# Kernel tuning notes

Measured on AMD Instinct MI355X. Metric: run time of the kernel, lower is better.

The kernel has to match this reference:

```python
import jax, jax.numpy as jnp
import numpy as np

NF = 128  # latent_dim / number of filters


def setup_inputs() -> dict:
    key = jax.random.key(0)
    k1, k2, k3, k4 = jax.random.split(key, 4)
    B, H, W, C = 4, 64, 64, 128
    x = jax.random.normal(k1, (B, H, W, C), dtype=jnp.float32)
    y = jax.random.normal(k2, (B, H, W, C), dtype=jnp.float32)
    # 1x1 conv kernels (C_in, C_out) + biases, glorot-ish scale
    scale = 1.0 / np.sqrt(C)
    W1 = jax.random.normal(k3, (C, NF), dtype=jnp.float32) * scale
    W2 = jax.random.normal(k4, (C, NF), dtype=jnp.float32) * scale
    b1 = jnp.zeros((NF,), dtype=jnp.float32)
    b2 = jnp.zeros((NF,), dtype=jnp.float32)
    return {"x": x, "y": y, "W1": W1, "b1": b1, "W2": W2, "b2": b2}


def reference(x, y, W1, b1, W2, b2):
    B, H, Wd, C = x.shape
    hw = H * Wd
    # 1x1 convs == per-pixel matmul
    xq = jnp.einsum('bhwc,cf->bhwf', x, W1) + b1   # conv1(x)
    yk = jnp.einsum('bhwc,cf->bhwf', y, W2) + b2   # conv2(y)
    xq_r = xq.reshape(B, hw, NF)
    yk_r = yk.reshape(B, hw, NF)
    # A_ij = sigmoid(y_i . x_j), full (hw x hw) sigmoid attention
    A = jax.nn.sigmoid(jnp.einsum('bic,bjc->bij', yk_r, xq_r))
    out = jnp.einsum('bij,bjc->bic', A, yk_r).reshape(B, H, Wd, NF)
    # residual add of the *projected* x (matches original: x was overwritten by conv1)
    out = out + xq
    return out
```

## Files before the change

### kernel.cpp

```cpp
#include <hip/hip_runtime.h>
#include <hip/hip_bf16.h>
#include <stdint.h>

typedef float f32x16 __attribute__((ext_vector_type(16)));
typedef float f32x4  __attribute__((ext_vector_type(4)));
typedef short s16x8  __attribute__((ext_vector_type(8)));
typedef unsigned int u32x4 __attribute__((ext_vector_type(4)));

#define HWSZ   4096
#define NBATCH 4
#define LOG2E  1.44269504088896340736f

__device__ __forceinline__ unsigned short f2bf(float f) {
    unsigned u = __builtin_bit_cast(unsigned, f);
    u += 0x7FFFu + ((u >> 16) & 1u);
    return (unsigned short)(u >> 16);
}
__device__ __forceinline__ unsigned cvt_pk_bf16(float lo, float hi) {
    __hip_bfloat162 h = __float22bfloat162_rn(make_float2(lo, hi));
    return *reinterpret_cast<unsigned*>(&h);
}
__device__ __forceinline__ float sigm2(float s) {
    return __builtin_amdgcn_rcpf(1.f + __builtin_amdgcn_exp2f(-s));
}
// ... 91 lines not shown
            for (int rg = 0; rg < 4; ++rg) {
                float p0 = acc[ft][4 * rg + 0] + bias_v[ft];
                float p1 = acc[ft][4 * rg + 1] + bias_v[ft];
                float p2 = acc[ft][4 * rg + 2] + bias_v[ft];
                float p3 = acc[ft][4 * rg + 3] + bias_v[ft];
                int jb = 8 * rg + 4 * g;
                *(uint2*)&Tlds[f][jb] = make_uint2(cvt_pk_bf16(p0, p1), cvt_pk_bf16(p2, p3));
                size_t o = (size_t)(r0 + jb) * 128 + f;
                yk_bf[o]       = f2bf(p0);
                yk_bf[o + 128] = f2bf(p1);
                yk_bf[o + 256] = f2bf(p2);
                yk_bf[o + 384] = f2bf(p3);
            }
        }
    }
    __syncthreads();

    {
        int f  = t >> 1;
        int jh = (t & 1) * 16;
        unsigned short* dst = ykT_bf + ((size_t)(b * 128 + f)) * HWSZ + j0 + jh;
        #pragma unroll
        for (int c = 0; c < 2; ++c)
            *(s16x8*)(dst + c * 8) = *(const s16x8*)&Tlds[f][jh + c * 8];
    }
}

#define KT_STR   136
#define VT_STR   72
#define KT_BYTES (64 * KT_STR * 2)
#define VT_BYTES (128 * VT_STR * 2)
#define BUF_BYTES (KT_BYTES + VT_BYTES)

__global__ __launch_bounds__(256, 2) void attn128_kernel(
    const unsigned short* __restrict__ Kbf,
    const unsigned short* __restrict__ Qbf,
    const unsigned short* __restrict__ Vtbf,
    unsigned* __restrict__ outp)
{
    __shared__ __align__(16) char smem[2 * BUF_BYTES];

    const int t    = threadIdx.x;
    const int lane = t & 63;
    const int qt   = t >> 6;
    const int l31  = lane & 31;
    const int g    = lane >> 5;

    const int split  = blockIdx.x >> 7;
    const int r      = blockIdx.x & 127;
    const int b      = r >> 5;
    const int qb     = (r & 31) * 128;
    const int jBegin = split * (HWSZ / 4);
    const int nt     = (HWSZ / 4) / 64;

    s16x8 qfrag[8];
    {
        const unsigned short* qp =
            Qbf + (((size_t)(b * HWSZ + qb + 32 * qt + l31)) << 7) + g * 8;
        #pragma unroll
        for (int fs = 0; fs < 8; ++fs)
            qfrag[fs] = *(const s16x8*)(qp + fs * 16);
    }

    f32x16 acc[4];
    #pragma unroll
    for (int ft = 0; ft < 4; ++ft)
        #pragma unroll
        for (int i = 0; i < 16; ++i) acc[ft][i] = 0.f;

    f32x16 zv;
    #pragma unroll
    for (int i = 0; i < 16; ++i) zv[i] = 0.f;

    const unsigned short* Kbase = Kbf  + (((size_t)b * HWSZ) << 7);
    const unsigned short* Vbase = Vtbf + (((size_t)b) << 7) * HWSZ;

    const unsigned short* kSrc = Kbase + (size_t)(jBegin + (t >> 4)) * 128 + (t & 15) * 8;
    const unsigned short* vSrc = Vbase + (size_t)(t >> 3) * HWSZ + jBegin + (t & 7) * 8;
    const int kDst = (t >> 4) * KT_STR + (t & 15) * 8;
    const int vDst = (t >> 3) * VT_STR + (t & 7) * 8;

    {
        unsigned short* Kl = (unsigned short*)smem;
        unsigned short* Vl = (unsigned short*)(smem + KT_BYTES);
        #pragma unroll
        for (int i = 0; i < 4; ++i)
            *(s16x8*)(Kl + kDst + i * 16 * KT_STR) = *(const s16x8*)(kSrc + (size_t)i * 2048);
        #pragma unroll
        for (int i = 0; i < 4; ++i)
            *(s16x8*)(Vl + vDst + i * 32 * VT_STR) = *(const s16x8*)(vSrc + (size_t)i * 32 * HWSZ);
    }
    __syncthreads();

    int c = 0;
    for (int it = 0; it < nt; ++it) {
        const bool pre = (it + 1 < nt);
        const unsigned short* Kl = (const unsigned short*)(smem + c * BUF_BYTES);
        const unsigned short* Vl = (const unsigned short*)(smem + c * BUF_BYTES + KT_BYTES);

        s16x8 kf0[8], kf1[8];
        {
            const unsigned short* Krow = Kl + (size_t)l31 * KT_STR + g * 8;
            #pragma unroll
            for (int fs = 0; fs < 8; ++fs)
                kf0[fs] = *(const s16x8*)(Krow + fs * 16);
        }
        f32x16 s0a, s0b;
        __builtin_amdgcn_s_setprio(1);
        #pragma unroll
        for (int fs = 0; fs < 4; ++fs) {
            s0a = __builtin_amdgcn_mfma_f32_32x32x16_bf16(kf0[fs],     qfrag[fs],
                      fs == 0 ? zv : s0a, 0, 0, 0);
            s0b = __builtin_amdgcn_mfma_f32_32x32x16_bf16(kf0[fs + 4], qfrag[fs + 4],
                      fs == 0 ? zv : s0b, 0, 0, 0);
        }
        __builtin_amdgcn_s_setprio(0);

        {
            const unsigned short* Krow = Kl + (size_t)(32 + l31) * KT_STR + g * 8;
            #pragma unroll
            for (int fs = 0; fs < 8; ++fs)
                kf1[fs] = *(const s16x8*)(Krow + fs * 16);
        }
        s16x8 kr[4], vr[4];
        if (pre) {
            kSrc += 64 * 128;
            vSrc += 64;
            #pragma unroll
            for (int i = 0; i < 4; ++i)
                kr[i] = *(const s16x8*)(kSrc + (size_t)i * 2048);
            #pragma unroll
            for (int i = 0; i < 4; ++i)
                vr[i] = *(const s16x8*)(vSrc + (size_t)i * 32 * HWSZ);
        }

        f32x16 s1a, s1b;
        unsigned W0[2][4], W1[2][4];
        #pragma unroll
        for (int fs = 0; fs < 4; ++fs) {
            s1a = __builtin_amdgcn_mfma_f32_32x32x16_bf16(kf1[fs],     qfrag[fs],
                      fs == 0 ? zv : s1a, 0, 0, 0);
            s1b = __builtin_amdgcn_mfma_f32_32x32x16_bf16(kf1[fs + 4], qfrag[fs + 4],
                      fs == 0 ? zv : s1b, 0, 0, 0);
            const int rg = fs;
            float p0 = sigm2(s0a[4 * rg + 0] + s0b[4 * rg + 0]);
            float p1 = sigm2(s0a[4 * rg + 1] + s0b[4 * rg + 1]);
            float p2 = sigm2(s0a[4 * rg + 2] + s0b[4 * rg + 2]);
            float p3 = sigm2(s0a[4 * rg + 3] + s0b[4 * rg + 3]);
            W0[0][rg] = cvt_pk_bf16(p0, p1);
            W1[0][rg] = cvt_pk_bf16(p2, p3);
        }

        __builtin_amdgcn_s_setprio(1);
        #pragma unroll
        for (int s2 = 0; s2 < 2; ++s2) {
            unsigned a0 = W0[0][2 * s2], b0 = W0[0][2 * s2 + 1];
            unsigned a1 = W1[0][2 * s2], b1 = W1[0][2 * s2 + 1];
            asm("v_permlane32_swap_b32 %0, %1" : "+v"(a0), "+v"(b0));
            asm("v_permlane32_swap_b32 %0, %1" : "+v"(a1), "+v"(b1));
            u32x4 pw;
            pw[0] = a0; pw[1] = a1; pw[2] = b0; pw[3] = b1;
            s16x8 pf = __builtin_bit_cast(s16x8, pw);
            #pragma unroll
            for (int ft = 0; ft < 4; ++ft) {
                s16x8 vf = *(const s16x8*)(Vl + (size_t)(32 * ft + l31) * VT_STR + s2 * 16 + g * 8);
                acc[ft] = __builtin_amdgcn_mfma_f32_32x32x16_bf16(pf, vf, acc[ft], 0, 0, 0);
            }
            #pragma unroll
            for (int h = 0; h < 2; ++h) {
                const int rg = 2 * s2 + h;
                float p0 = sigm2(s1a[4 * rg + 0] + s1b[4 * rg + 0]);
                float p1 = sigm2(s1a[4 * rg + 1] + s1b[4 * rg + 1]);
                float p2 = sigm2(s1a[4 * rg + 2] + s1b[4 * rg + 2]);
                float p3 = sigm2(s1a[4 * rg + 3] + s1b[4 * rg + 3]);
                W0[1][rg] = cvt_pk_bf16(p0, p1);
                W1[1][rg] = cvt_pk_bf16(p2, p3);
            }
        }

        #pragma unroll
        for (int s2 = 0; s2 < 2; ++s2) {
            unsigned a0 = W0[1][2 * s2], b0 = W0[1][2 * s2 + 1];
            unsigned a1 = W1[1][2 * s2], b1 = W1[1][2 * s2 + 1];
            asm("v_permlane32_swap_b32 %0, %1" : "+v"(a0), "+v"(b0));
            asm("v_permlane32_swap_b32 %0, %1" : "+v"(a1), "+v"(b1));
            u32x4 pw;
            pw[0] = a0; pw[1] = a1; pw[2] = b0; pw[3] = b1;
            s16x8 pf = __builtin_bit_cast(s16x8, pw);
            const int ks = 2 + s2;
            #pragma unroll
            for (int ft = 0; ft < 4; ++ft) {
                s16x8 vf = *(const s16x8*)(Vl + (size_t)(32 * ft + l31) * VT_STR + ks * 16 + g * 8);
                acc[ft] = __builtin_amdgcn_mfma_f32_32x32x16_bf16(pf, vf, acc[ft], 0, 0, 0);
            }
        }
        __builtin_amdgcn_s_setprio(0);

        if (pre) {
            unsigned short* Kd = (unsigned short*)(smem + (c ^ 1) * BUF_BYTES);
            unsigned short* Vd = (unsigned short*)(smem + (c ^ 1) * BUF_BYTES + KT_BYTES);
            #pragma unroll
            for (int i = 0; i < 4; ++i)
                *(s16x8*)(Kd + kDst + i * 16 * KT_STR) = kr[i];
            #pragma unroll
            for (int i = 0; i < 4; ++i)
                *(s16x8*)(Vd + vDst + i * 32 * VT_STR) = vr[i];
        }
        __syncthreads();
        c ^= 1;
    }

    unsigned* op = outp + (size_t)split * ((size_t)NBATCH * HWSZ * 64);
    #pragma unroll
    for (int ft = 0; ft < 4; ++ft)
    #pragma unroll
    for (int pr = 0; pr < 8; ++pr) {
        int r2 = 2 * pr;
        int row = (r2 & 3) + 8 * (r2 >> 2) + 4 * g;
        int q = qb + 32 * qt + row;
        unsigned v = cvt_pk_bf16(acc[ft][r2], acc[ft][r2 + 1]);
        op[((size_t)(b * HWSZ + q) >> 1) * 128 + 32 * ft + l31] = v;
    }
}

template<bool SPLIT>
__global__ __launch_bounds__(256, 2) void attn_kernel(
    const unsigned short* __restrict__ Kbf,
    const unsigned short* __restrict__ Qbf,
    const unsigned short* __restrict__ Vtbf,
    const float* __restrict__ resid,
    float* __restrict__ outp)
{
    __shared__ __align__(16) char smem[2 * BUF_BYTES];

    const int t    = threadIdx.x;
    const int lane = t & 63;
    const int w    = t >> 6;
    const int qt   = w & 1;
    const int jt   = w >> 1;
    const int l31  = lane & 31;
    const int g    = lane >> 5;

    int bid = blockIdx.x;
    int half = 0;
    if (SPLIT) { half = bid >> 8; bid &= 255; }
    const int b      = bid >> 6;
    const int qb     = (bid & 63) * 64;
    const int jBegin = half * (HWSZ / 2);
    const int nt     = (SPLIT ? HWSZ / 2 : HWSZ) / 64;

    s16x8 qfrag[8];
    {
        const unsigned short* qp =
            Qbf + (((size_t)(b * HWSZ + qb + 32 * qt + l31)) << 7) + g * 8;
        #pragma unroll
        for (int fs = 0; fs < 8; ++fs)
            qfrag[fs] = *(const s16x8*)(qp + fs * 16);
    }

    f32x16 acc[4];
    #pragma unroll
    for (int ft = 0; ft < 4; ++ft)
        #pragma unroll
        for (int i = 0; i < 16; ++i) acc[ft][i] = 0.f;

    const unsigned short* Kbase = Kbf  + (((size_t)b * HWSZ) << 7);
    const unsigned short* Vbase = Vtbf + (((size_t)b) << 7) * HWSZ;

    const unsigned short* kSrc = Kbase + (size_t)(jBegin + (t >> 4)) * 128 + (t & 15) * 8;
    const unsigned short* vSrc = Vbase + (size_t)(t >> 3) * HWSZ + jBegin + (t & 7) * 8;
    const int kDst = (t >> 4) * KT_STR + (t & 15) * 8;
    const int vDst = (t >> 3) * VT_STR + (t & 7) * 8;

    {
        unsigned short* Kl = (unsigned short*)smem;
        unsigned short* Vl = (unsigned short*)(smem + KT_BYTES);
        #pragma unroll
        for (int i = 0; i < 4; ++i)
            *(s16x8*)(Kl + kDst + i * 16 * KT_STR) = *(const s16x8*)(kSrc + (size_t)i * 2048);
        #pragma unroll
        for (int i = 0; i < 4; ++i)
            *(s16x8*)(Vl + vDst + i * 32 * VT_STR) = *(const s16x8*)(vSrc + (size_t)i * 32 * HWSZ);
    }
    __syncthreads();

    int c = 0;
    for (int it = 0; it < nt; ++it) {
        const bool pre = (it + 1 < nt);
        s16x8 kr[4], vr[4];
        if (pre) {
            kSrc += 64 * 128;
            vSrc += 64;
            #pragma unroll
            for (int i = 0; i < 4; ++i)
                kr[i] = *(const s16x8*)(kSrc + (size_t)i * 2048);
            #pragma unroll
            for (int i = 0; i < 4; ++i)
                vr[i] = *(const s16x8*)(vSrc + (size_t)i * 32 * HWSZ);
        }

        const unsigned short* Kl = (const unsigned short*)(smem + c * BUF_BYTES);
        const unsigned short* Vl = (const unsigned short*)(smem + c * BUF_BYTES + KT_BYTES);

        f32x16 sa, sb;
        #pragma unroll
        for (int i = 0; i < 16; ++i) { sa[i] = 0.f; sb[i] = 0.f; }
        const unsigned short* Krow = Kl + (size_t)(32 * jt + l31) * KT_STR + g * 8;
        __builtin_amdgcn_s_setprio(1);
        #pragma unroll
        for (int fs = 0; fs < 4; ++fs) {
            sa = __builtin_amdgcn_mfma_f32_32x32x16_bf16(
                     *(const s16x8*)(Krow + fs * 16), qfrag[fs], sa, 0, 0, 0);
            sb = __builtin_amdgcn_mfma_f32_32x32x16_bf16(
                     *(const s16x8*)(Krow + (fs + 4) * 16), qfrag[fs + 4], sb, 0, 0, 0);
        }
        __builtin_amdgcn_s_setprio(0);

        unsigned W0[4], W1[4];
        #pragma unroll
        for (int rg = 0; rg < 4; ++rg) {
            float p0 = sigm2(sa[4 * rg + 0] + sb[4 * rg + 0]);
            float p1 = sigm2(sa[4 * rg + 1] + sb[4 * rg + 1]);
            float p2 = sigm2(sa[4 * rg + 2] + sb[4 * rg + 2]);
            float p3 = sigm2(sa[4 * rg + 3] + sb[4 * rg + 3]);
            W0[rg] = cvt_pk_bf16(p0, p1);
            W1[rg] = cvt_pk_bf16(p2, p3);
        }

        #pragma unroll
        for (int s2 = 0; s2 < 2; ++s2) {
            unsigned a0 = W0[2 * s2], b0 = W0[2 * s2 + 1];
            unsigned a1 = W1[2 * s2], b1 = W1[2 * s2 + 1];
            asm("v_permlane32_swap_b32 %0, %1" : "+v"(a0), "+v"(b0));
            asm("v_permlane32_swap_b32 %0, %1" : "+v"(a1), "+v"(b1));
            u32x4 pw;
            pw[0] = a0; pw[1] = a1; pw[2] = b0; pw[3] = b1;
            s16x8 pf = __builtin_bit_cast(s16x8, pw);
            const int ks = 2 * jt + s2;
            __builtin_amdgcn_s_setprio(1);
            #pragma unroll
            for (int ft = 0; ft < 4; ++ft) {
                s16x8 vf = *(const s16x8*)(Vl + (size_t)(32 * ft + l31) * VT_STR + ks * 16 + g * 8);
                acc[ft] = __builtin_amdgcn_mfma_f32_32x32x16_bf16(pf, vf, acc[ft], 0, 0, 0);
            }
            __builtin_amdgcn_s_setprio(0);
        }

        if (pre) {
            unsigned short* Kd = (unsigned short*)(smem + (c ^ 1) * BUF_BYTES);
            unsigned short* Vd = (unsigned short*)(smem + (c ^ 1) * BUF_BYTES + KT_BYTES);
            #pragma unroll
            for (int i = 0; i < 4; ++i)
                *(s16x8*)(Kd + kDst + i * 16 * KT_STR) = kr[i];
            #pragma unroll
            for (int i = 0; i < 4; ++i)
                *(s16x8*)(Vd + vDst + i * 32 * VT_STR) = vr[i];
        }
        __syncthreads();
        c ^= 1;
    }

    float* red = (float*)smem;
    if (jt == 1) {
        #pragma unroll
        for (int ft = 0; ft < 4; ++ft)
        #pragma unroll
        for (int r = 0; r < 16; ++r) {
            int row = (r & 3) + 8 * (r >> 2) + 4 * g;
            red[qt * 4096 + row * 128 + 32 * ft + l31] = acc[ft][r];
        }
    }
    __syncthreads();
    if (jt == 0) {
        float* op = outp + (SPLIT ? (size_t)half * ((size_t)NBATCH * HWSZ * 128) : 0);
        #pragma unroll
        for (int ft = 0; ft < 4; ++ft)
        #pragma unroll
        for (int r = 0; r < 16; ++r) {
            int row = (r & 3) + 8 * (r >> 2) + 4 * g;
            float v = acc[ft][r] + red[qt * 4096 + row * 128 + 32 * ft + l31];
            int q = qb + 32 * qt + row;
            size_t o = (((size_t)(b * HWSZ + q)) << 7) + 32 * ft + l31;
            if (SPLIT) op[o] = v;
            else       op[o] = v + resid[o];
        }
    }
}

__global__ __launch_bounds__(256, 1) void reduce2_kernel(
    const float* __restrict__ p0, const float* __restrict__ p1, float* outp)
{
    int i = blockIdx.x * 256 + threadIdx.x;
    f32x4 a = ((const f32x4*)p0)[i];
    f32x4 b = ((const f32x4*)p1)[i];
    f32x4 c = ((f32x4*)outp)[i];
    ((f32x4*)outp)[i] = a + b + c;
}

__global__ __launch_bounds__(256, 1) void reduce4bf_kernel(
    const unsigned* __restrict__ parts, const unsigned short* __restrict__ xqu,
    float* __restrict__ outp)
{
    const size_t NU = (size_t)NBATCH * HWSZ * 64;
    size_t j0 = ((size_t)blockIdx.x * 256 + threadIdx.x) * 4;
    f32x4 lo, hi;
    #pragma unroll
    for (int e = 0; e < 4; ++e) { lo[e] = 0.f; hi[e] = 0.f; }
    #pragma unroll
    for (int k = 0; k < 4; ++k) {
        u32x4 v = *(const u32x4*)(parts + k * NU + j0);
        #pragma unroll
        for (int e = 0; e < 4; ++e) {
            lo[e] += bf_lo(v[e]);
            hi[e] += bf_hi(v[e]);
        }
    }
    size_t p  = j0 >> 7;
    int    f0 = (int)(j0 & 127);
    size_t o0 = (p * 2) * 128 + f0;
    const ushort4 r0 = *(const ushort4*)(xqu + o0);
    const ushort4 r1 = *(const ushort4*)(xqu + o0 + 128);
    lo[0] += bf2f(r0.x); lo[1] += bf2f(r0.y); lo[2] += bf2f(r0.z); lo[3] += bf2f(r0.w);
    hi[0] += bf2f(r1.x); hi[1] += bf2f(r1.y); hi[2] += bf2f(r1.z); hi[3] += bf2f(r1.w);
    *(f32x4*)(outp + o0)       = lo;
    *(f32x4*)(outp + o0 + 128) = hi;
}

extern "C" void kernel_launch(void* const* d_in, const int* in_sizes, int n_in,
                              void* d_out, int out_size, void* d_ws, size_t ws_size,
                              hipStream_t stream) {
    const float* x  = (const float*)d_in[0];
    const float* y  = (const float*)d_in[1];
    const float* W1 = (const float*)d_in[2];
    const float* b1 = (const float*)d_in[3];
    const float* W2 = (const float*)d_in[4];
    const float* b2 = (const float*)d_in[5];
    float* out = (float*)d_out;

    const size_t NELEM = (size_t)NBATCH * HWSZ * 128;
    unsigned short* xq_bf  = (unsigned short*)d_ws;
    unsigned short* yk_bf  = xq_bf + NELEM;
    unsigned short* ykT_bf = yk_bf + NELEM;
    unsigned short* xqu_bf = ykT_bf + NELEM;
    unsigned* partu = (unsigned*)(xqu_bf + NELEM);
    float* part = (float*)(ykT_bf + NELEM);

    if (ws_size >= NELEM * 16) {
        proj_kernel<false><<<(int)(NBATCH * HWSZ / 32), 256, 0, stream>>>(
            x, y, W1, b1, W2, b2, nullptr, xqu_bf, xq_bf, yk_bf, ykT_bf);
        attn128_kernel<<<512, 256, 0, stream>>>(xq_bf, yk_bf, ykT_bf, partu);
        reduce4bf_kernel<<<(int)(NELEM / 2048), 256, 0, stream>>>(partu, xqu_bf, out);
    } else if (ws_size >= NELEM * 14) {
        proj_kernel<true><<<(int)(NBATCH * HWSZ / 32), 256, 0, stream>>>(
            x, y, W1, b1, W2, b2, out, nullptr, xq_bf, yk_bf, ykT_bf);
        attn_kernel<true><<<512, 256, 0, stream>>>(xq_bf, yk_bf, ykT_bf, out, part);
        reduce2_kernel<<<(int)(NELEM / 1024), 256, 0, stream>>>(part, part + NELEM, out);
    } else {
        proj_kernel<true><<<(int)(NBATCH * HWSZ / 32), 256, 0, stream>>>(
            x, y, W1, b1, W2, b2, out, nullptr, xq_bf, yk_bf, ykT_bf);
        attn_kernel<false><<<256, 256, 0, stream>>>(xq_bf, yk_bf, ykT_bf, out, out);
    }
}
```

Measured before the change: 60.83 us.

## Process two query sub-tiles per wave in attention kernel to reuse K/V fragments

The 128-query attention block moves from four waves with one 32-row query tile each to two waves with two 32-row query tiles each. Each K fragment and V fragment read from LDS now feeds two MFMA chains, halving LDS reads per unit of work, and the S/sigmoid stages are interleaved across four score tiles to overlap exp with matrix ops. The cost is roughly double the accumulator and fragment registers per wave, a launch bound of one block, and half as many waves to hide latency, which may lower occupancy.

```diff
diff --git a/kernel.cpp b/kernel.cpp
--- a/kernel.cpp
+++ b/kernel.cpp
@@ -147,7 +147,7 @@
 #define VT_BYTES (128 * VT_STR * 2)
 #define BUF_BYTES (KT_BYTES + VT_BYTES)
 
-__global__ __launch_bounds__(256, 2) void attn128_kernel(
+__global__ __launch_bounds__(128, 1) void attn128w2_kernel(
     const unsigned short* __restrict__ Kbf,
     const unsigned short* __restrict__ Qbf,
     const unsigned short* __restrict__ Vtbf,
@@ -157,7 +157,7 @@
 
     const int t    = threadIdx.x;
     const int lane = t & 63;
-    const int qt   = t >> 6;
+    const int wv   = t >> 6;
     const int l31  = lane & 31;
     const int g    = lane >> 5;
 
@@ -168,20 +168,23 @@
     const int jBegin = split * (HWSZ / 4);
     const int nt     = (HWSZ / 4) / 64;
 
-    s16x8 qfrag[8];
-    {
+    s16x8 qfrag[2][8];
+    #pragma unroll
+    for (int qs = 0; qs < 2; ++qs) {
         const unsigned short* qp =
-            Qbf + (((size_t)(b * HWSZ + qb + 32 * qt + l31)) << 7) + g * 8;
+            Qbf + (((size_t)(b * HWSZ + qb + 64 * wv + 32 * qs + l31)) << 7) + g * 8;
         #pragma unroll
         for (int fs = 0; fs < 8; ++fs)
-            qfrag[fs] = *(const s16x8*)(qp + fs * 16);
-    }
-
-    f32x16 acc[4];
-    #pragma unroll
-    for (int ft = 0; ft < 4; ++ft)
-        #pragma unroll
-        for (int i = 0; i < 16; ++i) acc[ft][i] = 0.f;
+            qfrag[qs][fs] = *(const s16x8*)(qp + fs * 16);
+    }
+
+    f32x16 acc[2][4];
+    #pragma unroll
+    for (int qs = 0; qs < 2; ++qs)
+        #pragma unroll
+        for (int ft = 0; ft < 4; ++ft)
+            #pragma unroll
+            for (int i = 0; i < 16; ++i) acc[qs][ft][i] = 0.f;
 
     f32x16 zv;
     #pragma unroll
@@ -199,11 +202,11 @@
         unsigned short* Kl = (unsigned short*)smem;
         unsigned short* Vl = (unsigned short*)(smem + KT_BYTES);
         #pragma unroll
-        for (int i = 0; i < 4; ++i)
-            *(s16x8*)(Kl + kDst + i * 16 * KT_STR) = *(const s16x8*)(kSrc + (size_t)i * 2048);
-        #pragma unroll
-        for (int i = 0; i < 4; ++i)
-            *(s16x8*)(Vl + vDst + i * 32 * VT_STR) = *(const s16x8*)(vSrc + (size_t)i * 32 * HWSZ);
+        for (int i = 0; i < 8; ++i)
+            *(s16x8*)(Kl + kDst + i * 8 * KT_STR) = *(const s16x8*)(kSrc + (size_t)i * 1024);
+        #pragma unroll
+        for (int i = 0; i < 8; ++i)
+            *(s16x8*)(Vl + vDst + i * 16 * VT_STR) = *(const s16x8*)(vSrc + (size_t)i * 16 * HWSZ);
     }
     __syncthreads();
 
@@ -213,6 +216,8 @@
         const unsigned short* Kl = (const unsigned short*)(smem + c * BUF_BYTES);
         const unsigned short* Vl = (const unsigned short*)(smem + c * BUF_BYTES + KT_BYTES);
 
+        unsigned Wlo[2][2][4], Whi[2][2][4];
+
         s16x8 kf0[8], kf1[8];
         {
             const unsigned short* Krow = Kl + (size_t)l31 * KT_STR + g * 8;
@@ -220,14 +225,14 @@
             for (int fs = 0; fs < 8; ++fs)
                 kf0[fs] = *(const s16x8*)(Krow + fs * 16);
         }
-        f32x16 s0a, s0b;
+        f32x16 s00a, s00b;
         __builtin_amdgcn_s_setprio(1);
         #pragma unroll
         for (int fs = 0; fs < 4; ++fs) {
-            s0a = __builtin_amdgcn_mfma_f32_32x32x16_bf16(kf0[fs],     qfrag[fs],
-                      fs == 0 ? zv : s0a, 0, 0, 0);
-            s0b = __builtin_amdgcn_mfma_f32_32x32x16_bf16(kf0[fs + 4], qfrag[fs + 4],
-                      fs == 0 ? zv : s0b, 0, 0, 0);
+            s00a = __builtin_amdgcn_mfma_f32_32x32x16_bf16(kf0[fs],     qfrag[0][fs],
+                       fs == 0 ? zv : s00a, 0, 0, 0);
+            s00b = __builtin_amdgcn_mfma_f32_32x32x16_bf16(kf0[fs + 4], qfrag[0][fs + 4],
+                       fs == 0 ? zv : s00b, 0, 0, 0);
         }
         __builtin_amdgcn_s_setprio(0);
 
@@ -237,76 +242,119 @@
             for (int fs = 0; fs < 8; ++fs)
                 kf1[fs] = *(const s16x8*)(Krow + fs * 16);
         }
-        s16x8 kr[4], vr[4];
+        s16x8 kr[8], vr[8];
         if (pre) {
             kSrc += 64 * 128;
             vSrc += 64;
             #pragma unroll
-            for (int i = 0; i < 4; ++i)
-                kr[i] = *(const s16x8*)(kSrc + (size_t)i * 2048);
-            #pragma unroll
-            for (int i = 0; i < 4; ++i)
-                vr[i] = *(const s16x8*)(vSrc + (size_t)i * 32 * HWSZ);
-        }
-
-        f32x16 s1a, s1b;
-        unsigned W0[2][4], W1[2][4];
+            for (int i = 0; i < 8; ++i)
+                kr[i] = *(const s16x8*)(kSrc + (size_t)i * 1024);
+            #pragma unroll
+            for (int i = 0; i < 8; ++i)
+                vr[i] = *(const s16x8*)(vSrc + (size_t)i * 16 * HWSZ);
+        }
+
+        f32x16 s01a, s01b;
         #pragma unroll
         for (int fs = 0; fs < 4; ++fs) {
-            s1a = __builtin_amdgcn_mfma_f32_32x32x16_bf16(kf1[fs],     qfrag[fs],
-                      fs == 0 ? zv : s1a, 0, 0, 0);
-            s1b = __builtin_amdgcn_mfma_f32_32x32x16_bf16(kf1[fs + 4], qfrag[fs + 4],
-                      fs == 0 ? zv : s1b, 0, 0, 0);
+            s01a = __builtin_amdgcn_mfma_f32_32x32x16_bf16(kf0[fs],     qfrag[1][fs],
+                       fs == 0 ? zv : s01a, 0, 0, 0);
+            s01b = __builtin_amdgcn_mfma_f32_32x32x16_bf16(kf0[fs + 4], qfrag[1][fs + 4],
+                       fs == 0 ? zv : s01b, 0, 0, 0);
             const int rg = fs;
-            float p0 = sigm2(s0a[4 * rg + 0] + s0b[4 * rg + 0]);
-            float p1 = sigm2(s0a[4 * rg + 1] + s0b[4 * rg + 1]);
-            float p2 = sigm2(s0a[4 * rg + 2] + s0b[4 * rg + 2]);
-            float p3 = sigm2(s0a[4 * rg + 3] + s0b[4 * rg + 3]);
-            W0[0][rg] = cvt_pk_bf16(p0, p1);
-            W1[0][rg] = cvt_pk_bf16(p2, p3);
+            float p0 = sigm2(s00a[4 * rg + 0] + s00b[4 * rg + 0]);
+            float p1 = sigm2(s00a[4 * rg + 1] + s00b[4 * rg + 1]);
+            float p2 = sigm2(s00a[4 * rg + 2] + s00b[4 * rg + 2]);
+            float p3 = sigm2(s00a[4 * rg + 3] + s00b[4 * rg + 3]);
+            Wlo[0][0][rg] = cvt_pk_bf16(p0, p1);
+            Whi[0][0][rg] = cvt_pk_bf16(p2, p3);
+        }
+
+        f32x16 s10a, s10b;
+        #pragma unroll
+        for (int fs = 0; fs < 4; ++fs) {
+            s10a = __builtin_amdgcn_mfma_f32_32x32x16_bf16(kf1[fs],     qfrag[0][fs],
+                       fs == 0 ? zv : s10a, 0, 0, 0);
+            s10b = __builtin_amdgcn_mfma_f32_32x32x16_bf16(kf1[fs + 4], qfrag[0][fs + 4],
+                       fs == 0 ? zv : s10b, 0, 0, 0);
+            const int rg = fs;
+            float p0 = sigm2(s01a[4 * rg + 0] + s01b[4 * rg + 0]);
+            float p1 = sigm2(s01a[4 * rg + 1] + s01b[4 * rg + 1]);
+            float p2 = sigm2(s01a[4 * rg + 2] + s01b[4 * rg + 2]);
+            float p3 = sigm2(s01a[4 * rg + 3] + s01b[4 * rg + 3]);
+            Wlo[0][1][rg] = cvt_pk_bf16(p0, p1);
+            Whi[0][1][rg] = cvt_pk_bf16(p2, p3);
+        }
+
+        f32x16 s11a, s11b;
+        #pragma unroll
+        for (int fs = 0; fs < 4; ++fs) {
+            s11a = __builtin_amdgcn_mfma_f32_32x32x16_bf16(kf1[fs],     qfrag[1][fs],
+                       fs == 0 ? zv : s11a, 0, 0, 0);
+            s11b = __builtin_amdgcn_mfma_f32_32x32x16_bf16(kf1[fs + 4], qfrag[1][fs + 4],
+                       fs == 0 ? zv : s11b, 0, 0, 0);
+            const int rg = fs;
+            float p0 = sigm2(s10a[4 * rg + 0] + s10b[4 * rg + 0]);
+            float p1 = sigm2(s10a[4 * rg + 1] + s10b[4 * rg + 1]);
+            float p2 = sigm2(s10a[4 * rg + 2] + s10b[4 * rg + 2]);
+            float p3 = sigm2(s10a[4 * rg + 3] + s10b[4 * rg + 3]);
+            Wlo[1][0][rg] = cvt_pk_bf16(p0, p1);
+            Whi[1][0][rg] = cvt_pk_bf16(p2, p3);
         }
 
         __builtin_amdgcn_s_setprio(1);
         #pragma unroll
         for (int s2 = 0; s2 < 2; ++s2) {
-            unsigned a0 = W0[0][2 * s2], b0 = W0[0][2 * s2 + 1];
-            unsigned a1 = W1[0][2 * s2], b1 = W1[0][2 * s2 + 1];
+            unsigned a0 = Wlo[0][0][2 * s2], b0 = Wlo[0][0][2 * s2 + 1];
+            unsigned a1 = Whi[0][0][2 * s2], b1 = Whi[0][0][2 * s2 + 1];
             asm("v_permlane32_swap_b32 %0, %1" : "+v"(a0), "+v"(b0));
             asm("v_permlane32_swap_b32 %0, %1" : "+v"(a1), "+v"(b1));
-            u32x4 pw;
-            pw[0] = a0; pw[1] = a1; pw[2] = b0; pw[3] = b1;
-            s16x8 pf = __builtin_bit_cast(s16x8, pw);
+            u32x4 pw0; pw0[0] = a0; pw0[1] = a1; pw0[2] = b0; pw0[3] = b1;
+            s16x8 pf0 = __builtin_bit_cast(s16x8, pw0);
+            unsigned c0 = Wlo[0][1][2 * s2], d0 = Wlo[0][1][2 * s2 + 1];
+            unsigned c1 = Whi[0][1][2 * s2], d1 = Whi[0][1][2 * s2 + 1];
+            asm("v_permlane32_swap_b32 %0, %1" : "+v"(c0), "+v"(d0));
+            asm("v_permlane32_swap_b32 %0, %1" : "+v"(c1), "+v"(d1));
+            u32x4 pw1; pw1[0] = c0; pw1[1] = c1; pw1[2] = d0; pw1[3] = d1;
+            s16x8 pf1 = __builtin_bit_cast(s16x8, pw1);
             #pragma unroll
             for (int ft = 0; ft < 4; ++ft) {
                 s16x8 vf = *(const s16x8*)(Vl + (size_t)(32 * ft + l31) * VT_STR + s2 * 16 + g * 8);
-                acc[ft] = __builtin_amdgcn_mfma_f32_32x32x16_bf16(pf, vf, acc[ft], 0, 0, 0);
+                acc[0][ft] = __builtin_amdgcn_mfma_f32_32x32x16_bf16(pf0, vf, acc[0][ft], 0, 0, 0);
+                acc[1][ft] = __builtin_amdgcn_mfma_f32_32x32x16_bf16(pf1, vf, acc[1][ft], 0, 0, 0);
             }
             #pragma unroll
             for (int h = 0; h < 2; ++h) {
                 const int rg = 2 * s2 + h;
-                float p0 = sigm2(s1a[4 * rg + 0] + s1b[4 * rg + 0]);
-                float p1 = sigm2(s1a[4 * rg + 1] + s1b[4 * rg + 1]);
-                float p2 = sigm2(s1a[4 * rg + 2] + s1b[4 * rg + 2]);
-                float p3 = sigm2(s1a[4 * rg + 3] + s1b[4 * rg + 3]);
-                W0[1][rg] = cvt_pk_bf16(p0, p1);
-                W1[1][rg] = cvt_pk_bf16(p2, p3);
+                float p0 = sigm2(s11a[4 * rg + 0] + s11b[4 * rg + 0]);
+                float p1 = sigm2(s11a[4 * rg + 1] + s11b[4 * rg + 1]);
+                float p2 = sigm2(s11a[4 * rg + 2] + s11b[4 * rg + 2]);
+                float p3 = sigm2(s11a[4 * rg + 3] + s11b[4 * rg + 3]);
+                Wlo[1][1][rg] = cvt_pk_bf16(p0, p1);
+                Whi[1][1][rg] = cvt_pk_bf16(p2, p3);
             }
         }
 
         #pragma unroll
         for (int s2 = 0; s2 < 2; ++s2) {
-            unsigned a0 = W0[1][2 * s2], b0 = W0[1][2 * s2 + 1];
-            unsigned a1 = W1[1][2 * s2], b1 = W1[1][2 * s2 + 1];
+            unsigned a0 = Wlo[1][0][2 * s2], b0 = Wlo[1][0][2 * s2 + 1];
+            unsigned a1 = Whi[1][0][2 * s2], b1 = Whi[1][0][2 * s2 + 1];
             asm("v_permlane32_swap_b32 %0, %1" : "+v"(a0), "+v"(b0));
             asm("v_permlane32_swap_b32 %0, %1" : "+v"(a1), "+v"(b1));
-            u32x4 pw;
-            pw[0] = a0; pw[1] = a1; pw[2] = b0; pw[3] = b1;
-            s16x8 pf = __builtin_bit_cast(s16x8, pw);
+            u32x4 pw0; pw0[0] = a0; pw0[1] = a1; pw0[2] = b0; pw0[3] = b1;
+            s16x8 pf0 = __builtin_bit_cast(s16x8, pw0);
+            unsigned c0 = Wlo[1][1][2 * s2], d0 = Wlo[1][1][2 * s2 + 1];
+            unsigned c1 = Whi[1][1][2 * s2], d1 = Whi[1][1][2 * s2 + 1];
+            asm("v_permlane32_swap_b32 %0, %1" : "+v"(c0), "+v"(d0));
+            asm("v_permlane32_swap_b32 %0, %1" : "+v"(c1), "+v"(d1));
+            u32x4 pw1; pw1[0] = c0; pw1[1] = c1; pw1[2] = d0; pw1[3] = d1;
+            s16x8 pf1 = __builtin_bit_cast(s16x8, pw1);
             const int ks = 2 + s2;
             #pragma unroll
             for (int ft = 0; ft < 4; ++ft) {
                 s16x8 vf = *(const s16x8*)(Vl + (size_t)(32 * ft + l31) * VT_STR + ks * 16 + g * 8);
-                acc[ft] = __builtin_amdgcn_mfma_f32_32x32x16_bf16(pf, vf, acc[ft], 0, 0, 0);
+                acc[0][ft] = __builtin_amdgcn_mfma_f32_32x32x16_bf16(pf0, vf, acc[0][ft], 0, 0, 0);
+                acc[1][ft] = __builtin_amdgcn_mfma_f32_32x32x16_bf16(pf1, vf, acc[1][ft], 0, 0, 0);
             }
         }
         __builtin_amdgcn_s_setprio(0);
@@ -315,25 +363,27 @@
             unsigned short* Kd = (unsigned short*)(smem + (c ^ 1) * BUF_BYTES);
             unsigned short* Vd = (unsigned short*)(smem + (c ^ 1) * BUF_BYTES + KT_BYTES);
             #pragma unroll
-            for (int i = 0; i < 4; ++i)
-                *(s16x8*)(Kd + kDst + i * 16 * KT_STR) = kr[i];
-            #pragma unroll
-            for (int i = 0; i < 4; ++i)
-                *(s16x8*)(Vd + vDst + i * 32 * VT_STR) = vr[i];
+            for (int i = 0; i < 8; ++i)
+                *(s16x8*)(Kd + kDst + i * 8 * KT_STR) = kr[i];
+            #pragma unroll
+            for (int i = 0; i < 8; ++i)
+                *(s16x8*)(Vd + vDst + i * 16 * VT_STR) = vr[i];
         }
         __syncthreads();
         c ^= 1;
     }
 
     unsigned* op = outp + (size_t)split * ((size_t)NBATCH * HWSZ * 64);
+    #pragma unroll
+    for (int qs = 0; qs < 2; ++qs)
     #pragma unroll
     for (int ft = 0; ft < 4; ++ft)
     #pragma unroll
     for (int pr = 0; pr < 8; ++pr) {
         int r2 = 2 * pr;
         int row = (r2 & 3) + 8 * (r2 >> 2) + 4 * g;
-        int q = qb + 32 * qt + row;
-        unsigned v = cvt_pk_bf16(acc[ft][r2], acc[ft][r2 + 1]);
+        int q = qb + 64 * wv + 32 * qs + row;
+        unsigned v = cvt_pk_bf16(acc[qs][ft][r2], acc[qs][ft][r2 + 1]);
         op[((size_t)(b * HWSZ + q) >> 1) * 128 + 32 * ft + l31] = v;
     }
 }
@@ -563,7 +613,7 @@
     if (ws_size >= NELEM * 16) {
         proj_kernel<false><<<(int)(NBATCH * HWSZ / 32), 256, 0, stream>>>(
             x, y, W1, b1, W2, b2, nullptr, xqu_bf, xq_bf, yk_bf, ykT_bf);
-        attn128_kernel<<<512, 256, 0, stream>>>(xq_bf, yk_bf, ykT_bf, partu);
+        attn128w2_kernel<<<512, 128, 0, stream>>>(xq_bf, yk_bf, ykT_bf, partu);
         reduce4bf_kernel<<<(int)(NELEM / 2048), 256, 0, stream>>>(partu, xqu_bf, out);
     } else if (ws_size >= NELEM * 14) {
         proj_kernel<true><<<(int)(NBATCH * HWSZ / 32), 256, 0, stream>>>(
```

New measurement: 68.51 us. 1.13x slower.

## Load K fragments directly from global into registers, dropping K LDS staging

Applied to the files above, without the earlier changes.

K tiles are no longer staged through shared memory. Each wave now reads its K MFMA fragments straight from global memory into registers and prefetches the next tile's fragments mid-iteration. This removes the K writes to LDS and the later LDS reads, and shrinks shared memory to the V buffers only. In exchange, every one of the 4 waves in a block loads the same K data from global memory (4x redundant traffic, relying on L2/cache hits), and holding 16 extra fragment registers raises register pressure and could hurt occupancy at launch_bounds(256,2).

```diff
diff --git a/kernel.cpp b/kernel.cpp
--- a/kernel.cpp
+++ b/kernel.cpp
@@ -153,7 +153,7 @@
     const unsigned short* __restrict__ Vtbf,
     unsigned* __restrict__ outp)
 {
-    __shared__ __align__(16) char smem[2 * BUF_BYTES];
+    __shared__ __align__(16) unsigned short Vlds[2][128 * VT_STR];
 
     const int t    = threadIdx.x;
     const int lane = t & 63;
@@ -190,60 +190,45 @@
     const unsigned short* Kbase = Kbf  + (((size_t)b * HWSZ) << 7);
     const unsigned short* Vbase = Vtbf + (((size_t)b) << 7) * HWSZ;
 
-    const unsigned short* kSrc = Kbase + (size_t)(jBegin + (t >> 4)) * 128 + (t & 15) * 8;
+    const unsigned short* kPtr = Kbase + (size_t)(jBegin + l31) * 128 + g * 8;
+
+    s16x8 kf[16];
+    #pragma unroll
+    for (int jt = 0; jt < 2; ++jt)
+        #pragma unroll
+        for (int fs = 0; fs < 8; ++fs)
+            kf[jt * 8 + fs] = *(const s16x8*)(kPtr + jt * 32 * 128 + fs * 16);
+
     const unsigned short* vSrc = Vbase + (size_t)(t >> 3) * HWSZ + jBegin + (t & 7) * 8;
-    const int kDst = (t >> 4) * KT_STR + (t & 15) * 8;
     const int vDst = (t >> 3) * VT_STR + (t & 7) * 8;
 
     {
-        unsigned short* Kl = (unsigned short*)smem;
-        unsigned short* Vl = (unsigned short*)(smem + KT_BYTES);
         #pragma unroll
         for (int i = 0; i < 4; ++i)
-            *(s16x8*)(Kl + kDst + i * 16 * KT_STR) = *(const s16x8*)(kSrc + (size_t)i * 2048);
-        #pragma unroll
-        for (int i = 0; i < 4; ++i)
-            *(s16x8*)(Vl + vDst + i * 32 * VT_STR) = *(const s16x8*)(vSrc + (size_t)i * 32 * HWSZ);
+            *(s16x8*)(&Vlds[0][0] + vDst + i * 32 * VT_STR) =
+                *(const s16x8*)(vSrc + (size_t)i * 32 * HWSZ);
     }
     __syncthreads();
 
     int c = 0;
     for (int it = 0; it < nt; ++it) {
         const bool pre = (it + 1 < nt);
-        const unsigned short* Kl = (const unsigned short*)(smem + c * BUF_BYTES);
-        const unsigned short* Vl = (const unsigned short*)(smem + c * BUF_BYTES + KT_BYTES);
-
-        s16x8 kf0[8], kf1[8];
-        {
-            const unsigned short* Krow = Kl + (size_t)l31 * KT_STR + g * 8;
-            #pragma unroll
-            for (int fs = 0; fs < 8; ++fs)
-                kf0[fs] = *(const s16x8*)(Krow + fs * 16);
-        }
+        const unsigned short* Vl = &Vlds[c][0];
+
         f32x16 s0a, s0b;
         __builtin_amdgcn_s_setprio(1);
         #pragma unroll
         for (int fs = 0; fs < 4; ++fs) {
-            s0a = __builtin_amdgcn_mfma_f32_32x32x16_bf16(kf0[fs],     qfrag[fs],
+            s0a = __builtin_amdgcn_mfma_f32_32x32x16_bf16(kf[fs],     qfrag[fs],
                       fs == 0 ? zv : s0a, 0, 0, 0);
-            s0b = __builtin_amdgcn_mfma_f32_32x32x16_bf16(kf0[fs + 4], qfrag[fs + 4],
+            s0b = __builtin_amdgcn_mfma_f32_32x32x16_bf16(kf[fs + 4], qfrag[fs + 4],
                       fs == 0 ? zv : s0b, 0, 0, 0);
         }
         __builtin_amdgcn_s_setprio(0);
 
-        {
-            const unsigned short* Krow = Kl + (size_t)(32 + l31) * KT_STR + g * 8;
-            #pragma unroll
-            for (int fs = 0; fs < 8; ++fs)
-                kf1[fs] = *(const s16x8*)(Krow + fs * 16);
-        }
-        s16x8 kr[4], vr[4];
+        s16x8 vr[4];
         if (pre) {
-            kSrc += 64 * 128;
             vSrc += 64;
-            #pragma unroll
-            for (int i = 0; i < 4; ++i)
-                kr[i] = *(const s16x8*)(kSrc + (size_t)i * 2048);
             #pragma unroll
             for (int i = 0; i < 4; ++i)
                 vr[i] = *(const s16x8*)(vSrc + (size_t)i * 32 * HWSZ);
@@ -253,9 +238,9 @@
         unsigned W0[2][4], W1[2][4];
         #pragma unroll
         for (int fs = 0; fs < 4; ++fs) {
-            s1a = __builtin_amdgcn_mfma_f32_32x32x16_bf16(kf1[fs],     qfrag[fs],
+            s1a = __builtin_amdgcn_mfma_f32_32x32x16_bf16(kf[8 + fs],     qfrag[fs],
                       fs == 0 ? zv : s1a, 0, 0, 0);
-            s1b = __builtin_amdgcn_mfma_f32_32x32x16_bf16(kf1[fs + 4], qfrag[fs + 4],
+            s1b = __builtin_amdgcn_mfma_f32_32x32x16_bf16(kf[8 + fs + 4], qfrag[fs + 4],
                       fs == 0 ? zv : s1b, 0, 0, 0);
             const int rg = fs;
             float p0 = sigm2(s0a[4 * rg + 0] + s0b[4 * rg + 0]);
@@ -264,6 +249,15 @@
             float p3 = sigm2(s0a[4 * rg + 3] + s0b[4 * rg + 3]);
             W0[0][rg] = cvt_pk_bf16(p0, p1);
             W1[0][rg] = cvt_pk_bf16(p2, p3);
+        }
+
+        if (pre) {
+            kPtr += 64 * 128;
+            #pragma unroll
+            for (int jt = 0; jt < 2; ++jt)
+                #pragma unroll
+                for (int fs = 0; fs < 8; ++fs)
+                    kf[jt * 8 + fs] = *(const s16x8*)(kPtr + jt * 32 * 128 + fs * 16);
         }
 
         __builtin_amdgcn_s_setprio(1);
@@ -312,14 +306,9 @@
         __builtin_amdgcn_s_setprio(0);
 
         if (pre) {
-            unsigned short* Kd = (unsigned short*)(smem + (c ^ 1) * BUF_BYTES);
-            unsigned short* Vd = (unsigned short*)(smem + (c ^ 1) * BUF_BYTES + KT_BYTES);
             #pragma unroll
             for (int i = 0; i < 4; ++i)
-                *(s16x8*)(Kd + kDst + i * 16 * KT_STR) = kr[i];
-            #pragma unroll
-            for (int i = 0; i < 4; ++i)
-                *(s16x8*)(Vd + vDst + i * 32 * VT_STR) = vr[i];
+                *(s16x8*)(&Vlds[c ^ 1][0] + vDst + i * 32 * VT_STR) = vr[i];
         }
         __syncthreads();
         c ^= 1;
```

New measurement: 86.54 us. +42.3%, slower.

## Add six-way key-split attention kernel with single-buffered LDS and pipelined sigmoid

Applied to the files above, without the earlier changes.

Adds attn6_kernel, which splits the key/value dimension six ways (768 blocks of 11 or 10 tiles) instead of four, and targets three blocks per CU by dropping to a single LDS buffer. Inside the loop it computes the two 32-row score tiles one after the other and overlaps the sigmoid of the first with the score MFMAs of the second. It also overlaps the second sigmoid with the PV MFMAs of the first. The reduce kernel is templated on the split count, and the older fp32 fallback paths are removed. The new path needs a larger workspace, and the extra split adds partial-output traffic in the reduce. The single buffer also adds an extra barrier per tile.

```diff
diff --git a/kernel.cpp b/kernel.cpp
--- a/kernel.cpp
+++ b/kernel.cpp
@@ -147,6 +147,189 @@
 #define VT_BYTES (128 * VT_STR * 2)
 #define BUF_BYTES (KT_BYTES + VT_BYTES)
 
+__global__ __launch_bounds__(256, 3) void attn6_kernel(
+    const unsigned short* __restrict__ Kbf,
+    const unsigned short* __restrict__ Qbf,
+    const unsigned short* __restrict__ Vtbf,
+    unsigned* __restrict__ outp)
+{
+    __shared__ __align__(16) unsigned short Klds[64 * KT_STR];
+    __shared__ __align__(16) unsigned short Vlds[128 * VT_STR];
+
+    const int t    = threadIdx.x;
+    const int lane = t & 63;
+    const int qt   = t >> 6;
+    const int l31  = lane & 31;
+    const int g    = lane >> 5;
+
+    const int split = blockIdx.x >> 7;
+    const int r     = blockIdx.x & 127;
+    const int b     = r >> 5;
+    const int qb    = (r & 31) * 128;
+    const int st    = 11 * split - (split > 4 ? split - 4 : 0);
+    const int nt    = (split >= 4) ? 10 : 11;
+    const int jBegin = st * 64;
+
+    s16x8 qfrag[8];
+    {
+        const unsigned short* qp =
+            Qbf + (((size_t)(b * HWSZ + qb + 32 * qt + l31)) << 7) + g * 8;
+        #pragma unroll
+        for (int fs = 0; fs < 8; ++fs)
+            qfrag[fs] = *(const s16x8*)(qp + fs * 16);
+    }
+
+    f32x16 acc[4];
+    #pragma unroll
+    for (int ft = 0; ft < 4; ++ft)
+        #pragma unroll
+        for (int i = 0; i < 16; ++i) acc[ft][i] = 0.f;
+
+    f32x16 zv;
+    #pragma unroll
+    for (int i = 0; i < 16; ++i) zv[i] = 0.f;
+
+    const unsigned short* Kbase = Kbf  + (((size_t)b * HWSZ) << 7);
+    const unsigned short* Vbase = Vtbf + (((size_t)b) << 7) * HWSZ;
+
+    const unsigned short* kSrc = Kbase + (size_t)(jBegin + (t >> 4)) * 128 + (t & 15) * 8;
+    const unsigned short* vSrc = Vbase + (size_t)(t >> 3) * HWSZ + jBegin + (t & 7) * 8;
+    const int kDst = (t >> 4) * KT_STR + (t & 15) * 8;
+    const int vDst = (t >> 3) * VT_STR + (t & 7) * 8;
+
+    {
+        #pragma unroll
+        for (int i = 0; i < 4; ++i)
+            *(s16x8*)(Klds + kDst + i * 16 * KT_STR) = *(const s16x8*)(kSrc + (size_t)i * 2048);
+        #pragma unroll
+        for (int i = 0; i < 4; ++i)
+            *(s16x8*)(Vlds + vDst + i * 32 * VT_STR) = *(const s16x8*)(vSrc + (size_t)i * 32 * HWSZ);
+    }
+    __syncthreads();
+
+    for (int it = 0; it < nt; ++it) {
+        const bool pre = (it + 1 < nt);
+
+        s16x8 kf0[8], kf1[8];
+        {
+            const unsigned short* Krow = Klds + (size_t)l31 * KT_STR + g * 8;
+            #pragma unroll
+            for (int fs = 0; fs < 8; ++fs)
+                kf0[fs] = *(const s16x8*)(Krow + fs * 16);
+        }
+        f32x16 s0;
+        __builtin_amdgcn_s_setprio(1);
+        #pragma unroll
+        for (int fs = 0; fs < 8; ++fs)
+            s0 = __builtin_amdgcn_mfma_f32_32x32x16_bf16(kf0[fs], qfrag[fs],
+                     fs == 0 ? zv : s0, 0, 0, 0);
+        __builtin_amdgcn_s_setprio(0);
+
+        {
+            const unsigned short* Krow = Klds + (size_t)(32 + l31) * KT_STR + g * 8;
+            #pragma unroll
+            for (int fs = 0; fs < 8; ++fs)
+                kf1[fs] = *(const s16x8*)(Krow + fs * 16);
+        }
+        s16x8 kr[4], vr[4];
+        if (pre) {
+            kSrc += 64 * 128;
+            vSrc += 64;
+            #pragma unroll
+            for (int i = 0; i < 4; ++i)
+                kr[i] = *(const s16x8*)(kSrc + (size_t)i * 2048);
+            #pragma unroll
+            for (int i = 0; i < 4; ++i)
+                vr[i] = *(const s16x8*)(vSrc + (size_t)i * 32 * HWSZ);
+        }
+
+        f32x16 s1;
+        unsigned W0[2][4], W1[2][4];
+        #pragma unroll
+        for (int fs = 0; fs < 8; ++fs) {
+            s1 = __builtin_amdgcn_mfma_f32_32x32x16_bf16(kf1[fs], qfrag[fs],
+                     fs == 0 ? zv : s1, 0, 0, 0);
+            if (fs < 4) {
+                const int rg = fs;
+                float p0 = sigm2(s0[4 * rg + 0]);
+                float p1 = sigm2(s0[4 * rg + 1]);
+                float p2 = sigm2(s0[4 * rg + 2]);
+                float p3 = sigm2(s0[4 * rg + 3]);
+                W0[0][rg] = cvt_pk_bf16(p0, p1);
+                W1[0][rg] = cvt_pk_bf16(p2, p3);
+            }
+        }
+
+        __builtin_amdgcn_s_setprio(1);
+        #pragma unroll
+        for (int s2 = 0; s2 < 2; ++s2) {
+            unsigned a0 = W0[0][2 * s2], b0 = W0[0][2 * s2 + 1];
+            unsigned a1 = W1[0][2 * s2], b1 = W1[0][2 * s2 + 1];
+            asm("v_permlane32_swap_b32 %0, %1" : "+v"(a0), "+v"(b0));
+            asm("v_permlane32_swap_b32 %0, %1" : "+v"(a1), "+v"(b1));
+            u32x4 pw;
+            pw[0] = a0; pw[1] = a1; pw[2] = b0; pw[3] = b1;
+            s16x8 pf = __builtin_bit_cast(s16x8, pw);
+            #pragma unroll
+            for (int ft = 0; ft < 4; ++ft) {
+                s16x8 vf = *(const s16x8*)(Vlds + (size_t)(32 * ft + l31) * VT_STR + s2 * 16 + g * 8);
+                acc[ft] = __builtin_amdgcn_mfma_f32_32x32x16_bf16(pf, vf, acc[ft], 0, 0, 0);
+            }
+            #pragma unroll
+            for (int h = 0; h < 2; ++h) {
+                const int rg = 2 * s2 + h;
+                float p0 = sigm2(s1[4 * rg + 0]);
+                float p1 = sigm2(s1[4 * rg + 1]);
+                float p2 = sigm2(s1[4 * rg + 2]);
+                float p3 = sigm2(s1[4 * rg + 3]);
+                W0[1][rg] = cvt_pk_bf16(p0, p1);
+                W1[1][rg] = cvt_pk_bf16(p2, p3);
+            }
+        }
+
+        #pragma unroll
+        for (int s2 = 0; s2 < 2; ++s2) {
+            unsigned a0 = W0[1][2 * s2], b0 = W0[1][2 * s2 + 1];
+            unsigned a1 = W1[1][2 * s2], b1 = W1[1][2 * s2 + 1];
+            asm("v_permlane32_swap_b32 %0, %1" : "+v"(a0), "+v"(b0));
+            asm("v_permlane32_swap_b32 %0, %1" : "+v"(a1), "+v"(b1));
+            u32x4 pw;
+            pw[0] = a0; pw[1] = a1; pw[2] = b0; pw[3] = b1;
+            s16x8 pf = __builtin_bit_cast(s16x8, pw);
+            const int ks = 2 + s2;
+            #pragma unroll
+            for (int ft = 0; ft < 4; ++ft) {
+                s16x8 vf = *(const s16x8*)(Vlds + (size_t)(32 * ft + l31) * VT_STR + ks * 16 + g * 8);
+                acc[ft] = __builtin_amdgcn_mfma_f32_32x32x16_bf16(pf, vf, acc[ft], 0, 0, 0);
+            }
+        }
+        __builtin_amdgcn_s_setprio(0);
+
+        __syncthreads();
+        if (pre) {
+            #pragma unroll
+            for (int i = 0; i < 4; ++i)
+                *(s16x8*)(Klds + kDst + i * 16 * KT_STR) = kr[i];
+            #pragma unroll
+            for (int i = 0; i < 4; ++i)
+                *(s16x8*)(Vlds + vDst + i * 32 * VT_STR) = vr[i];
+            __syncthreads();
+        }
+    }
+
+    unsigned* op = outp + (size_t)split * ((size_t)NBATCH * HWSZ * 64);
+    #pragma unroll
+    for (int ft = 0; ft < 4; ++ft)
+    #pragma unroll
+    for (int pr = 0; pr < 8; ++pr) {
+        int r2 = 2 * pr;
+        int row = (r2 & 3) + 8 * (r2 >> 2) + 4 * g;
+        int q = qb + 32 * qt + row;
+        unsigned v = cvt_pk_bf16(acc[ft][r2], acc[ft][r2 + 1]);
+        op[((size_t)(b * HWSZ + q) >> 1) * 128 + 32 * ft + l31] = v;
+    }
+}
+
 __global__ __launch_bounds__(256, 2) void attn128_kernel(
     const unsigned short* __restrict__ Kbf,
     const unsigned short* __restrict__ Qbf,
@@ -338,181 +521,8 @@
     }
 }
 
-template<bool SPLIT>
-__global__ __launch_bounds__(256, 2) void attn_kernel(
-    const unsigned short* __restrict__ Kbf,
-    const unsigned short* __restrict__ Qbf,
-    const unsigned short* __restrict__ Vtbf,
-    const float* __restrict__ resid,
-    float* __restrict__ outp)
-{
-    __shared__ __align__(16) char smem[2 * BUF_BYTES];
-
-    const int t    = threadIdx.x;
-    const int lane = t & 63;
-    const int w    = t >> 6;
-    const int qt   = w & 1;
-    const int jt   = w >> 1;
-    const int l31  = lane & 31;
-    const int g    = lane >> 5;
-
-    int bid = blockIdx.x;
-    int half = 0;
-    if (SPLIT) { half = bid >> 8; bid &= 255; }
-    const int b      = bid >> 6;
-    const int qb     = (bid & 63) * 64;
-    const int jBegin = half * (HWSZ / 2);
-    const int nt     = (SPLIT ? HWSZ / 2 : HWSZ) / 64;
-
-    s16x8 qfrag[8];
-    {
-        const unsigned short* qp =
-            Qbf + (((size_t)(b * HWSZ + qb + 32 * qt + l31)) << 7) + g * 8;
-        #pragma unroll
-        for (int fs = 0; fs < 8; ++fs)
-            qfrag[fs] = *(const s16x8*)(qp + fs * 16);
-    }
-
-    f32x16 acc[4];
-    #pragma unroll
-    for (int ft = 0; ft < 4; ++ft)
-        #pragma unroll
-        for (int i = 0; i < 16; ++i) acc[ft][i] = 0.f;
-
-    const unsigned short* Kbase = Kbf  + (((size_t)b * HWSZ) << 7);
-    const unsigned short* Vbase = Vtbf + (((size_t)b) << 7) * HWSZ;
-
-    const unsigned short* kSrc = Kbase + (size_t)(jBegin + (t >> 4)) * 128 + (t & 15) * 8;
-    const unsigned short* vSrc = Vbase + (size_t)(t >> 3) * HWSZ + jBegin + (t & 7) * 8;
-    const int kDst = (t >> 4) * KT_STR + (t & 15) * 8;
-    const int vDst = (t >> 3) * VT_STR + (t & 7) * 8;
-
-    {
-        unsigned short* Kl = (unsigned short*)smem;
-        unsigned short* Vl = (unsigned short*)(smem + KT_BYTES);
-        #pragma unroll
-        for (int i = 0; i < 4; ++i)
-            *(s16x8*)(Kl + kDst + i * 16 * KT_STR) = *(const s16x8*)(kSrc + (size_t)i * 2048);
-        #pragma unroll
-        for (int i = 0; i < 4; ++i)
-            *(s16x8*)(Vl + vDst + i * 32 * VT_STR) = *(const s16x8*)(vSrc + (size_t)i * 32 * HWSZ);
-    }
-    __syncthreads();
-
-    int c = 0;
-    for (int it = 0; it < nt; ++it) {
-        const bool pre = (it + 1 < nt);
-        s16x8 kr[4], vr[4];
-        if (pre) {
-            kSrc += 64 * 128;
-            vSrc += 64;
-            #pragma unroll
-            for (int i = 0; i < 4; ++i)
-                kr[i] = *(const s16x8*)(kSrc + (size_t)i * 2048);
-            #pragma unroll
-            for (int i = 0; i < 4; ++i)
-                vr[i] = *(const s16x8*)(vSrc + (size_t)i * 32 * HWSZ);
-        }
-
-        const unsigned short* Kl = (const unsigned short*)(smem + c * BUF_BYTES);
-        const unsigned short* Vl = (const unsigned short*)(smem + c * BUF_BYTES + KT_BYTES);
-
-        f32x16 sa, sb;
-        #pragma unroll
-        for (int i = 0; i < 16; ++i) { sa[i] = 0.f; sb[i] = 0.f; }
-        const unsigned short* Krow = Kl + (size_t)(32 * jt + l31) * KT_STR + g * 8;
-        __builtin_amdgcn_s_setprio(1);
-        #pragma unroll
-        for (int fs = 0; fs < 4; ++fs) {
-            sa = __builtin_amdgcn_mfma_f32_32x32x16_bf16(
-                     *(const s16x8*)(Krow + fs * 16), qfrag[fs], sa, 0, 0, 0);
-            sb = __builtin_amdgcn_mfma_f32_32x32x16_bf16(
-                     *(const s16x8*)(Krow + (fs + 4) * 16), qfrag[fs + 4], sb, 0, 0, 0);
-        }
-        __builtin_amdgcn_s_setprio(0);
-
-        unsigned W0[4], W1[4];
-        #pragma unroll
-        for (int rg = 0; rg < 4; ++rg) {
-            float p0 = sigm2(sa[4 * rg + 0] + sb[4 * rg + 0]);
-            float p1 = sigm2(sa[4 * rg + 1] + sb[4 * rg + 1]);
-            float p2 = sigm2(sa[4 * rg + 2] + sb[4 * rg + 2]);
-            float p3 = sigm2(sa[4 * rg + 3] + sb[4 * rg + 3]);
-            W0[rg] = cvt_pk_bf16(p0, p1);
-            W1[rg] = cvt_pk_bf16(p2, p3);
-        }
-
-        #pragma unroll
-        for (int s2 = 0; s2 < 2; ++s2) {
-            unsigned a0 = W0[2 * s2], b0 = W0[2 * s2 + 1];
-            unsigned a1 = W1[2 * s2], b1 = W1[2 * s2 + 1];
-            asm("v_permlane32_swap_b32 %0, %1" : "+v"(a0), "+v"(b0));
-            asm("v_permlane32_swap_b32 %0, %1" : "+v"(a1), "+v"(b1));
-            u32x4 pw;
-            pw[0] = a0; pw[1] = a1; pw[2] = b0; pw[3] = b1;
-            s16x8 pf = __builtin_bit_cast(s16x8, pw);
-            const int ks = 2 * jt + s2;
-            __builtin_amdgcn_s_setprio(1);
-            #pragma unroll
-            for (int ft = 0; ft < 4; ++ft) {
-                s16x8 vf = *(const s16x8*)(Vl + (size_t)(32 * ft + l31) * VT_STR + ks * 16 + g * 8);
-                acc[ft] = __builtin_amdgcn_mfma_f32_32x32x16_bf16(pf, vf, acc[ft], 0, 0, 0);
-            }
-            __builtin_amdgcn_s_setprio(0);
-        }
-
-        if (pre) {
-            unsigned short* Kd = (unsigned short*)(smem + (c ^ 1) * BUF_BYTES);
-            unsigned short* Vd = (unsigned short*)(smem + (c ^ 1) * BUF_BYTES + KT_BYTES);
-            #pragma unroll
-            for (int i = 0; i < 4; ++i)
-                *(s16x8*)(Kd + kDst + i * 16 * KT_STR) = kr[i];
-            #pragma unroll
-            for (int i = 0; i < 4; ++i)
-                *(s16x8*)(Vd + vDst + i * 32 * VT_STR) = vr[i];
-        }
-        __syncthreads();
-        c ^= 1;
-    }
-
-    float* red = (float*)smem;
-    if (jt == 1) {
-        #pragma unroll
-        for (int ft = 0; ft < 4; ++ft)
-        #pragma unroll
-        for (int r = 0; r < 16; ++r) {
-            int row = (r & 3) + 8 * (r >> 2) + 4 * g;
-            red[qt * 4096 + row * 128 + 32 * ft + l31] = acc[ft][r];
-        }
-    }
-    __syncthreads();
-    if (jt == 0) {
-        float* op = outp + (SPLIT ? (size_t)half * ((size_t)NBATCH * HWSZ * 128) : 0);
-        #pragma unroll
-        for (int ft = 0; ft < 4; ++ft)
-        #pragma unroll
-        for (int r = 0; r < 16; ++r) {
-            int row = (r & 3) + 8 * (r >> 2) + 4 * g;
-            float v = acc[ft][r] + red[qt * 4096 + row * 128 + 32 * ft + l31];
-            int q = qb + 32 * qt + row;
-            size_t o = (((size_t)(b * HWSZ + q)) << 7) + 32 * ft + l31;
-            if (SPLIT) op[o] = v;
-            else       op[o] = v + resid[o];
-        }
-    }
-}
-
-__global__ __launch_bounds__(256, 1) void reduce2_kernel(
-    const float* __restrict__ p0, const float* __restrict__ p1, float* outp)
-{
-    int i = blockIdx.x * 256 + threadIdx.x;
-    f32x4 a = ((const f32x4*)p0)[i];
-    f32x4 b = ((const f32x4*)p1)[i];
-    f32x4 c = ((f32x4*)outp)[i];
-    ((f32x4*)outp)[i] = a + b + c;
-}
-
-__global__ __launch_bounds__(256, 1) void reduce4bf_kernel(
+template<int S>
+__global__ __launch_bounds__(256, 1) void reduceSbf_kernel(
     const unsigned* __restrict__ parts, const unsigned short* __restrict__ xqu,
     float* __restrict__ outp)
 {
@@ -522,7 +532,7 @@
     #pragma unroll
     for (int e = 0; e < 4; ++e) { lo[e] = 0.f; hi[e] = 0.f; }
     #pragma unroll
-    for (int k = 0; k < 4; ++k) {
+    for (int k = 0; k < S; ++k) {
         u32x4 v = *(const u32x4*)(parts + k * NU + j0);
         #pragma unroll
         for (int e = 0; e < 4; ++e) {
@@ -558,21 +568,21 @@
     unsigned short* ykT_bf = yk_bf + NELEM;
     unsigned short* xqu_bf = ykT_bf + NELEM;
     unsigned* partu = (unsigned*)(xqu_bf + NELEM);
-    float* part = (float*)(ykT_bf + NELEM);
-
-    if (ws_size >= NELEM * 16) {
+
+    if (ws_size >= NELEM * 20) {
+        proj_kernel<false><<<(int)(NBATCH * HWSZ / 32), 256, 0, stream>>>(
+            x, y, W1, b1, W2, b2, nullptr, xqu_bf, xq_bf, yk_bf, ykT_bf);
+        attn6_kernel<<<768, 256, 0, stream>>>(xq_bf, yk_bf, ykT_bf, partu);
+        reduceSbf_kernel<6><<<(int)(NELEM / 2048), 256, 0, stream>>>(partu, xqu_bf, out);
+    } else if (ws_size >= NELEM * 16) {
         proj_kernel<false><<<(int)(NBATCH * HWSZ / 32), 256, 0, stream>>>(
             x, y, W1, b1, W2, b2, nullptr, xqu_bf, xq_bf, yk_bf, ykT_bf);
         attn128_kernel<<<512, 256, 0, stream>>>(xq_bf, yk_bf, ykT_bf, partu);
-        reduce4bf_kernel<<<(int)(NELEM / 2048), 256, 0, stream>>>(partu, xqu_bf, out);
-    } else if (ws_size >= NELEM * 14) {
-        proj_kernel<true><<<(int)(NBATCH * HWSZ / 32), 256, 0, stream>>>(
-            x, y, W1, b1, W2, b2, out, nullptr, xq_bf, yk_bf, ykT_bf);
-        attn_kernel<true><<<512, 256, 0, stream>>>(xq_bf, yk_bf, ykT_bf, out, part);
-        reduce2_kernel<<<(int)(NELEM / 1024), 256, 0, stream>>>(part, part + NELEM, out);
+        reduceSbf_kernel<4><<<(int)(NELEM / 2048), 256, 0, stream>>>(partu, xqu_bf, out);
     } else {
-        proj_kernel<true><<<(int)(NBATCH * HWSZ / 32), 256, 0, stream>>>(
-            x, y, W1, b1, W2, b2, out, nullptr, xq_bf, yk_bf, ykT_bf);
-        attn_kernel<false><<<256, 256, 0, stream>>>(xq_bf, yk_bf, ykT_bf, out, out);
-    }
-}
+        proj_kernel<false><<<(int)(NBATCH * HWSZ / 32), 256, 0, stream>>>(
+            x, y, W1, b1, W2, b2, nullptr, xqu_bf, xq_bf, yk_bf, ykT_bf);
+        attn128_kernel<<<512, 256, 0, stream>>>(xq_bf, yk_bf, ykT_bf, partu);
+        reduceSbf_kernel<4><<<(int)(NELEM / 2048), 256, 0, stream>>>(partu, xqu_bf, out);
+    }
+}
```

After: 152.0 us. +149.9%, slower.
